# Optimization experiments

Measured on AMD Instinct MI355X. Metric: run time of the kernel, lower is better.

Reference implementation:

```python
import jax, jax.numpy as jnp
import numpy as np

NG, NR, C = 50000, 12000, 128     # lane nodes, roi nodes, n_map
NS = 6                            # num_scales
EPS, ELR, E1, E2 = 50000, 5000, 150000, 150000
GN_EPS = 1e-5


def gn(x, sb):
    # GroupNorm(num_groups=1) on [N, C]: normalize over C per row (biased var)
    m = x.mean(-1, keepdims=True)
    v = x.var(-1, keepdims=True)
    return (x - m) / jnp.sqrt(v + GN_EPS) * sb[0] + sb[1]


def lane_pooling(ctx_feat, ctx_pose, tgt_feat, tgt_pose, hi, wi,
                 input_w, relpose_w, relpose_b, ctx1_w, ctx1_gn, ctx2_w,
                 mlp1_w, mlp1_gn, mlp2_w, mlp2_gn, norm_gn):
    dist_feat = jax.nn.relu((ctx_pose[hi] - tgt_pose[wi]) @ relpose_w.T + relpose_b)  # [E,128]
    ctx = jnp.concatenate([ctx_feat[hi], dist_feat], -1)                               # [E,256]
    ctx = jax.nn.relu(gn(ctx @ ctx1_w.T, ctx1_gn)) @ ctx2_w.T                          # [E,128]
    identity = tgt_feat
    t = tgt_feat @ input_w.T
    t = t.at[wi].add(ctx)                 # scatter-reduce onto target nodes
    t = jax.nn.relu(gn(t, norm_gn))
    t = jax.nn.relu(gn(t @ mlp1_w.T, mlp1_gn))
    t = gn(t @ mlp2_w.T, mlp2_gn)
    return jax.nn.relu(t + identity)


def global_graph(feat, ps_u, ps_v, lr_u, lr_v,
                 ctr_w, ps_w, left_w, right_w, norm_gn, ctr2_w, ctr2_gn):
    res = feat
    for i in range(4):  # 4 fusion layers (structurally distinct weights)
        temp = feat @ ctr_w[i].T
        for k in range(2 * NS):  # pre0..pre5, suc0..suc5
            temp = temp.at[ps_u[k]].add(feat[ps_v[k]] @ ps_w[i, k].T)
        temp = temp.at[lr_u[0]].add(feat[lr_v[0]] @ left_w[i].T)
        temp = temp.at[lr_u[1]].add(feat[lr_v[1]] @ right_w[i].T)
        feat = jax.nn.relu(gn(temp, norm_gn[i]))
        feat = gn(feat @ ctr2_w[i].T, ctr2_gn[i])
        feat = jax.nn.relu(feat + res)
        res = feat
    return feat


def _gn_pack(key, lead):
    k1, k2 = jax.random.split(key)
    scale = 1.0 + 0.1 * jax.random.normal(k1, lead + (C,), jnp.float32)
    bias = 0.1 * jax.random.normal(k2, lead + (C,), jnp.float32)
    return jnp.stack([scale, bias], axis=-2)  # [..., 2, C]


def setup_inputs() -> dict:
    key = jax.random.key(0)
    ks = jax.random.split(key, 32)
    w = lambda k, sh: 0.05 * jax.random.normal(k, sh, jnp.float32)
    inp = {
        'roi_feat': jax.random.normal(ks[0], (NR, C), jnp.float32),
        'graph_pose': jax.random.normal(ks[1], (NG, 4), jnp.float32),
        'roi_pose': jax.random.normal(ks[2], (NR, 4), jnp.float32),
        'lp_input_w': w(ks[3], (2, C, C)),
        'lp_relpose_w': w(ks[4], (2, C, 4)),
        'lp_relpose_b': w(ks[5], (2, C)),
        'lp_ctx1_w': w(ks[6], (2, C, 2 * C)),
        'lp_ctx1_gn': _gn_pack(ks[7], (2,)),
        'lp_ctx2_w': w(ks[8], (2, C, C)),
        'lp_mlp1_w': w(ks[9], (2, C, C)),
        'lp_mlp1_gn': _gn_pack(ks[10], (2,)),
        'lp_mlp2_w': w(ks[11], (2, C, C)),
        'lp_mlp2_gn': _gn_pack(ks[12], (2,)),
        'lp_norm_gn': _gn_pack(ks[13], (2,)),
        'fuse_ctr_w': w(ks[14], (4, C, C)),
        'fuse_ps_w': w(ks[15], (4, 2 * NS, C, C)),
        'fuse_left_w': w(ks[16], (4, C, C)),
        'fuse_right_w': w(ks[17], (4, C, C)),
        'fuse_norm_gn': _gn_pack(ks[18], (4,)),
        'fuse_ctr2_w': w(ks[19], (4, C, C)),
        'fuse_ctr2_gn': _gn_pack(ks[20], (4,)),
        'e1_hi': jax.random.randint(ks[21], (E1,), 0, NR, jnp.int32),
        'e1_wi': jax.random.randint(ks[22], (E1,), 0, NG, jnp.int32),
        'e2_hi': jax.random.randint(ks[23], (E2,), 0, NG, jnp.int32),
        'e2_wi': jax.random.randint(ks[24], (E2,), 0, NR, jnp.int32),
        'ps_u': jax.random.randint(ks[25], (2 * NS, EPS), 0, NG, jnp.int32),
        'ps_v': jax.random.randint(ks[26], (2 * NS, EPS), 0, NG, jnp.int32),
        'lr_u': jax.random.randint(ks[27], (2, ELR), 0, NG, jnp.int32),
        'lr_v': jax.random.randint(ks[28], (2, ELR), 0, NG, jnp.int32),
    }
    return inp


def reference(roi_feat, graph_pose, roi_pose, lp_input_w, lp_relpose_w, lp_relpose_b,
              lp_ctx1_w, lp_ctx1_gn, lp_ctx2_w, lp_mlp1_w, lp_mlp1_gn, lp_mlp2_w,
              lp_mlp2_gn, lp_norm_gn, fuse_ctr_w, fuse_ps_w, fuse_left_w, fuse_right_w,
              fuse_norm_gn, fuse_ctr2_w, fuse_ctr2_gn, e1_hi, e1_wi, e2_hi, e2_wi,
              ps_u, ps_v, lr_u, lr_v):
    lp = lambda j: (lp_input_w[j], lp_relpose_w[j], lp_relpose_b[j], lp_ctx1_w[j],
                    lp_ctx1_gn[j], lp_ctx2_w[j], lp_mlp1_w[j], lp_mlp1_gn[j],
                    lp_mlp2_w[j], lp_mlp2_gn[j], lp_norm_gn[j])
    graph_feat = jnp.zeros((NG, C), jnp.float32)
    # roi2graph: context = roi, target = graph
    graph_feat = lane_pooling(roi_feat, roi_pose, graph_feat, graph_pose, e1_hi, e1_wi, *lp(0))
    graph_feat = global_graph(graph_feat, ps_u, ps_v, lr_u, lr_v,
                              fuse_ctr_w, fuse_ps_w, fuse_left_w, fuse_right_w,
                              fuse_norm_gn, fuse_ctr2_w, fuse_ctr2_gn)
    # graph2roi: context = graph, target = roi
    out = lane_pooling(graph_feat, graph_pose, roi_feat, roi_pose, e2_hi, e2_wi, *lp(1))
    return out
```

## Files before the change

kernel.cpp:

```cpp
#include <hip/hip_runtime.h>

#define NG 50000
#define NR 12000
#define EPS_N 50000
#define ELR_N 5000
#define E1_N 150000
#define E2_N 150000
#define GN_EPS_F 1e-5f
#define SCAN_CHUNK 4096
#define WST 136

typedef __attribute__((ext_vector_type(8))) __bf16 bf16x8;
typedef __attribute__((ext_vector_type(4))) float f32x4;

__device__ __forceinline__ bf16x8 cvt8(const float* __restrict__ p) {
    float4 x0 = *reinterpret_cast<const float4*>(p);
    float4 x1 = *reinterpret_cast<const float4*>(p + 4);
    bf16x8 a;
    a[0] = (__bf16)x0.x; a[1] = (__bf16)x0.y; a[2] = (__bf16)x0.z; a[3] = (__bf16)x0.w;
    a[4] = (__bf16)x1.x; a[5] = (__bf16)x1.y; a[6] = (__bf16)x1.z; a[7] = (__bf16)x1.w;
    return a;
}

struct PrepTab { const float* src[80]; int stride[80]; int n; };

__global__ void prepw_k(PrepTab tab, __bf16* __restrict__ wbuf)
{
    int t = blockIdx.x * 256 + threadIdx.x;
    int w = t >> 11;
    if (w >= tab.n) return;
    int rr = t & 2047;
    int chunk = rr >> 6, l = rr & 63;
    int wn = chunk >> 4, ks = (chunk >> 2) & 3, ni = chunk & 3;
    int c = wn * 64 + ni * 16 + (l & 15);
    int kb = (ks * 4 + (l >> 4)) * 8;
    const float* s = tab.src[w] + (size_t)c * tab.stride[w] + kb;
    bf16x8 o;
    #pragma unroll
    for (int e = 0; e < 8; ++e) o[e] = (__bf16)s[e];
    *reinterpret_cast<bf16x8*>(wbuf + (size_t)w * 16384 + rr * 8) = o;
}

__global__ void hist14_k(const int* __restrict__ ps_u, const int* __restrict__ lr_u,
                         int* __restrict__ cnt)
{
    int t = blockIdx.x * 256 + threadIdx.x;
    const int total = 12 * EPS_N + 2 * ELR_N;
    if (t >= total) return;
    int k, u;
    if (t < 12 * EPS_N) { k = t / EPS_N; u = ps_u[t]; }
    else { int r = t - 12 * EPS_N; k = 12 + r / ELR_N; u = lr_u[r]; }
    atomicAdd(&cnt[k * NG + u], 1);
}

__global__ void fill14_k(const int* __restrict__ ps_u, const int* __restrict__ ps_v,
                         const int* __restrict__ lr_u, const int* __restrict__ lr_v,
                         int* __restrict__ head, int* __restrict__ col)
{
    int t = blockIdx.x * 256 + threadIdx.x;
    const int total = 12 * EPS_N + 2 * ELR_N;
    if (t >= total) return;
    int k, u, v;
    if (t < 12 * EPS_N) { k = t / EPS_N; u = ps_u[t]; v = ps_v[t]; }
    else { int r = t - 12 * EPS_N; k = 12 + r / ELR_N; u = lr_u[r]; v = lr_v[r]; }
    int pos = atomicAdd(&head[k * NG + u], 1);
    col[pos] = v;
}

__global__ void histE_k(const int* __restrict__ wi, int n, int* __restrict__ cnt)
{
    int t = blockIdx.x * 256 + threadIdx.x;
    if (t >= n) return;
    atomicAdd(&cnt[wi[t]], 1);
}

__global__ void fillE_k(const int* __restrict__ wi, int n,
                        int* __restrict__ head, int* __restrict__ col)
{
    int t = blockIdx.x * 256 + threadIdx.x;
    if (t >= n) return;
    int pos = atomicAdd(&head[wi[t]], 1);
    col[pos] = t;
}

__global__ void scan1_k(const int* __restrict__ in, int n, int* __restrict__ bsum)
{
    __shared__ int sm[4];
    int base = blockIdx.x * SCAN_CHUNK;
    int s = 0;
    for (int i = threadIdx.x; i < SCAN_CHUNK; i += 256) {
        int idx = base + i;
        s += (idx < n) ? in[idx] : 0;
    }
    #pragma unroll
    for (int off = 1; off < 64; off <<= 1) s += __shfl_xor(s, off);
    if ((threadIdx.x & 63) == 0) sm[threadIdx.x >> 6] = s;
    __syncthreads();
    if (threadIdx.x == 0) bsum[blockIdx.x] = sm[0] + sm[1] + sm[2] + sm[3];
}

__global__ void scan2_k(int* __restrict__ bsum, int nb)
{
    if (threadIdx.x == 0) {
        int acc = 0;
        for (int i = 0; i < nb; ++i) { int t = bsum[i]; bsum[i] = acc; acc += t; }
    }
}

__global__ void scan3_k(const int* __restrict__ in, int n,
                        const int* __restrict__ bsum, int* __restrict__ outp)
{
    __shared__ int sm[256];
    int base = blockIdx.x * SCAN_CHUNK;
    int loc[16]; int s = 0;
    #pragma unroll
    for (int i = 0; i < 16; ++i) {
        int idx = base + threadIdx.x * 16 + i;
        loc[i] = (idx < n) ? in[idx] : 0; s += loc[i];
    }
    sm[threadIdx.x] = s; __syncthreads();
    for (int off = 1; off < 256; off <<= 1) {
        int v = (threadIdx.x >= off) ? sm[threadIdx.x - off] : 0;
        __syncthreads();
        sm[threadIdx.x] += v;
        __syncthreads();
    }
    int tp = (threadIdx.x ? sm[threadIdx.x - 1] : 0) + bsum[blockIdx.x];
    #pragma unroll
    for (int i = 0; i < 16; ++i) {
        int idx = base + threadIdx.x * 16 + i;
        if (idx < n) outp[idx] = tp;
        tp += loc[i];
        if (idx == n - 1) outp[n] = tp;
    }
}


__device__ __forceinline__ void mfma16(f32x4 (&acc)[8], const bf16x8 (&a)[4],
                                       const __bf16* __restrict__ gw, int lane)
{
    const __bf16* gwb = gw + lane * 8;
    #pragma unroll
    for (int ks = 0; ks < 4; ++ks) {
        #pragma unroll
        for (int n2 = 0; n2 < 8; ++n2) {
            const int chunk = (n2 >> 2) * 16 + ks * 4 + (n2 & 3);
            bf16x8 b = *reinterpret_cast<const bf16x8*>(gwb + chunk * 512);
            acc[n2] = __builtin_amdgcn_mfma_f32_16x16x32_bf16(a[ks], b, acc[n2], 0, 0, 0);
        }
    }
}

__device__ __forceinline__ void ss_to_frags(const float (&ss)[32], bf16x8 (&a)[4])
{
    #pragma unroll
    for (int ks = 0; ks < 4; ++ks)
        #pragma unroll
        for (int i = 0; i < 8; ++i)
            a[ks][i] = (__bf16)ss[ks * 8 + i];
}

__device__ __forceinline__ void gn_mi(const f32x4 (&acc)[8], float (&m)[4], float (&inv)[4])
{
    #pragma unroll
    for (int reg = 0; reg < 4; ++reg) {
        float s = 0.f, q = 0.f;
        #pragma unroll
        for (int n2 = 0; n2 < 8; ++n2) { float v = acc[n2][reg]; s += v; q = fmaf(v, v, q); }
        #pragma unroll
        for (int off = 1; off < 16; off <<= 1) {
            s += __shfl_xor(s, off);
            q += __shfl_xor(q, off);
        }
        m[reg] = s * (1.f / 128.f);
        inv[reg] = rsqrtf(fmaxf(q * (1.f / 128.f) - m[reg] * m[reg], 0.f) + GN_EPS_F);
    }
}

__device__ __forceinline__ void gn_relayout(const f32x4 (&acc)[8], const float* __restrict__ sb,
                                            __bf16* wl, bf16x8 (&a)[4], int r16, int kq)
{
    float m[4], inv[4];
    gn_mi(acc, m, inv);
    #pragma unroll
    for (int reg = 0; reg < 4; ++reg) {
        #pragma unroll
        for (int n2 = 0; n2 < 8; ++n2) {
            const int colc = n2 * 16 + r16;
            float y = (acc[n2][reg] - m[reg]) * inv[reg] * sb[colc] + sb[128 + colc];
            wl[(kq * 4 + reg) * WST + colc] = (__bf16)fmaxf(y, 0.f);
        }
    }
    #pragma unroll
    for (int ks = 0; ks < 4; ++ks)
        a[ks] = *reinterpret_cast<const bf16x8*>(wl + r16 * WST + ks * 32 + kq * 8);
}

template<typename CT>
__launch_bounds__(128, 3)
__global__ void edgefull_k(const int* __restrict__ hi_idx, const int* __restrict__ wi_idx,
                           const CT* __restrict__ ctxfeat,
                           const float* __restrict__ cpose, const float* __restrict__ tpose,
                           const float* __restrict__ rpw, const float* __restrict__ rpb,
                           const __bf16* __restrict__ wc1A, const __bf16* __restrict__ wc1B,
                           const float* __restrict__ sb,
                           __bf16* __restrict__ hout, int M)
{
    __shared__ float rw[640];
    const int tid = threadIdx.x, lane = tid & 63, wv = tid >> 6;
    const int r16 = lane & 15, kq = lane >> 4;
    const int wbase = blockIdx.x * 32 + wv * 16;
    const int erow = wbase + r16;
    const int ec = erow < M ? erow : M - 1;

    for (int i = tid; i < 640; i += 128)
        rw[i] = (i < 512) ? rpw[i] : rpb[i - 512];
    __syncthreads();

    const int hi = hi_idx[ec], wi = wi_idx[ec];
    float4 cp = *reinterpret_cast<const float4*>(cpose + (size_t)hi * 4);
    float4 tp = *reinterpret_cast<const float4*>(tpose + (size_t)wi * 4);
    const float d0 = cp.x - tp.x, d1 = cp.y - tp.y, d2 = cp.z - tp.z, d3 = cp.w - tp.w;

    f32x4 acc[8];
    #pragma unroll
    for (int n2 = 0; n2 < 8; ++n2) acc[n2] = (f32x4){0.f, 0.f, 0.f, 0.f};

    {
        bf16x8 a[4];
        const CT* sp = ctxfeat + (size_t)hi * 128 + kq * 8;
        #pragma unroll
        for (int ks = 0; ks < 4; ++ks) {
            if constexpr (sizeof(CT) == 4) a[ks] = cvt8((const float*)sp + ks * 32);
            else a[ks] = *reinterpret_cast<const bf16x8*>((const __bf16*)sp + ks * 32);
        }
        mfma16(acc, a, wc1A, lane);
    }
    {
        bf16x8 a[4];
        #pragma unroll
        for (int ks = 0; ks < 4; ++ks)
            #pragma unroll
            for (int i = 0; i < 8; ++i) {
                const int k = ks * 32 + kq * 8 + i;
                float4 w4 = *reinterpret_cast<const float4*>(&rw[k * 4]);
                float d = fmaf(d0, w4.x, fmaf(d1, w4.y, fmaf(d2, w4.z,
                          fmaf(d3, w4.w, rw[512 + k]))));
                a[ks][i] = (__bf16)fmaxf(d, 0.f);
            }
        mfma16(acc, a, wc1B, lane);
    }

    float m[4], inv[4];
    gn_mi(acc, m, inv);
    #pragma unroll
    for (int reg = 0; reg < 4; ++reg) {
        const int crow = wbase + kq * 4 + reg;
        if (crow < M) {
            __bf16* dp = hout + (size_t)crow * 128 + r16;
            #pragma unroll
            for (int n2 = 0; n2 < 8; ++n2) {
                const int colc = n2 * 16 + r16;
                float y = (acc[n2][reg] - m[reg]) * inv[reg] * sb[colc] + sb[128 + colc];
                dp[n2 * 16] = (__bf16)fmaxf(y, 0.f);
            }
        }
    }
}

struct FW { const __bf16* w[16]; };

__launch_bounds__(128, 3)
__global__ void fusedlayer_k(const __bf16* __restrict__ feat,
                             const int* __restrict__ rp, const int* __restrict__ col,
                             FW fw, const float* __restrict__ gn1,
                             const float* __restrict__ gn2,
                             __bf16* __restrict__ outp, int M)
{
    __shared__ __bf16 wl[2][16 * WST];
    const int tid = threadIdx.x, lane = tid & 63, wv = tid >> 6;
    const int r16 = lane & 15, kq = lane >> 4;
    const int wbase = blockIdx.x * 32 + wv * 16;
    const int wrow = (wbase + r16) < M ? (wbase + r16) : M - 1;

    f32x4 acc[8];
    #pragma unroll
    for (int n2 = 0; n2 < 8; ++n2) acc[n2] = (f32x4){0.f, 0.f, 0.f, 0.f};

    #pragma unroll
    for (int j = 0; j < 15; ++j) {
        float ss[32];
        #pragma unroll
        for (int i = 0; i < 32; ++i) ss[i] = 0.f;
        if (j == 14) {
            const __bf16* sp = feat + (size_t)wrow * 128 + kq * 8;
            #pragma unroll
            for (int ks = 0; ks < 4; ++ks) {
                bf16x8 h = *reinterpret_cast<const bf16x8*>(sp + ks * 32);
                #pragma unroll
                for (int i = 0; i < 8; ++i) ss[ks * 8 + i] = (float)h[i];
            }
        } else {
            const int b = rp[j * M + wrow], e = rp[j * M + wrow + 1];
            for (int t2 = b; t2 < e; ++t2) {
                const __bf16* sp = feat + (size_t)col[t2] * 128 + kq * 8;
                #pragma unroll
                for (int ks = 0; ks < 4; ++ks) {
                    bf16x8 h = *reinterpret_cast<const bf16x8*>(sp + ks * 32);
                    #pragma unroll
                    for (int i = 0; i < 8; ++i) ss[ks * 8 + i] += (float)h[i];
                }
            }
        }
        bf16x8 a[4];
        ss_to_frags(ss, a);
        mfma16(acc, a, fw.w[j], lane);
    }

    bf16x8 a2[4];
    gn_relayout(acc, gn1, wl[wv], a2, r16, kq);
    f32x4 acc2[8];
    #pragma unroll
    for (int n2 = 0; n2 < 8; ++n2) acc2[n2] = (f32x4){0.f, 0.f, 0.f, 0.f};
    mfma16(acc2, a2, fw.w[15], lane);

    float m[4], inv[4];
    gn_mi(acc2, m, inv);
    #pragma unroll
    for (int reg = 0; reg < 4; ++reg) {
        const int crow = wbase + kq * 4 + reg;
        if (crow < M) {
            __bf16* dp = outp + (size_t)crow * 128 + r16;
            const __bf16* rs = feat + (size_t)crow * 128 + r16;
            #pragma unroll
            for (int n2 = 0; n2 < 8; ++n2) {
                const int colc = n2 * 16 + r16;
                float y = (acc2[n2][reg] - m[reg]) * inv[reg] * gn2[colc] + gn2[128 + colc];
                y += (float)rs[n2 * 16];
                dp[n2 * 16] = (__bf16)fmaxf(y, 0.f);
            }
        }
    }
}

template<bool LP2>
__launch_bounds__(128, 3)
__global__ void lptail_k(const __bf16* __restrict__ hsrc,
                         const int* __restrict__ rp, const int* __restrict__ col,
                         const float* __restrict__ roi,
                         const __bf16* __restrict__ wc2, const __bf16* __restrict__ winW,
                         const __bf16* __restrict__ wm1, const __bf16* __restrict__ wm2,
                         const float* __restrict__ ngn, const float* __restrict__ m1gn,
                         const float* __restrict__ m2gn,
                         void* __restrict__ outp, int M)
{
    __shared__ __bf16 wl[2][16 * WST];
    const int tid = threadIdx.x, lane = tid & 63, wv = tid >> 6;
    const int r16 = lane & 15, kq = lane >> 4;
    const int wbase = blockIdx.x * 32 + wv * 16;
    const int wrow = (wbase + r16) < M ? (wbase + r16) : M - 1;

    f32x4 acc[8];
    #pragma unroll
    for (int n2 = 0; n2 < 8; ++n2) acc[n2] = (f32x4){0.f, 0.f, 0.f, 0.f};

    {
        float ss[32];
        #pragma unroll
        for (int i = 0; i < 32; ++i) ss[i] = 0.f;
        const int b = rp[wrow], e = rp[wrow + 1];
        for (int t2 = b; t2 < e; ++t2) {
            const __bf16* sp = hsrc + (size_t)col[t2] * 128 + kq * 8;
            #pragma unroll
            for (int ks = 0; ks < 4; ++ks) {
                bf16x8 h = *reinterpret_cast<const bf16x8*>(sp + ks * 32);
                #pragma unroll
                for (int i = 0; i < 8; ++i) ss[ks * 8 + i] += (float)h[i];
            }
        }
        bf16x8 a[4];
        ss_to_frags(ss, a);
        mfma16(acc, a, wc2, lane);
    }
    if (LP2) {
        bf16x8 a[4];
        const float* sp = roi + (size_t)wrow * 128 + kq * 8;
        #pragma unroll
        for (int ks = 0; ks < 4; ++ks) a[ks] = cvt8(sp + ks * 32);
        mfma16(acc, a, winW, lane);
    }

    {
        bf16x8 a[4];
        gn_relayout(acc, ngn, wl[wv], a, r16, kq);
        #pragma unroll
        for (int n2 = 0; n2 < 8; ++n2) acc[n2] = (f32x4){0.f, 0.f, 0.f, 0.f};
        mfma16(acc, a, wm1, lane);
    }
    {
        bf16x8 a[4];
        gn_relayout(acc, m1gn, wl[wv], a, r16, kq);
        #pragma unroll
        for (int n2 = 0; n2 < 8; ++n2) acc[n2] = (f32x4){0.f, 0.f, 0.f, 0.f};
        mfma16(acc, a, wm2, lane);
    }

    float m[4], inv[4];
    gn_mi(acc, m, inv);
    #pragma unroll
    for (int reg = 0; reg < 4; ++reg) {
        const int crow = wbase + kq * 4 + reg;
        if (crow < M) {
            #pragma unroll
            for (int n2 = 0; n2 < 8; ++n2) {
                const int colc = n2 * 16 + r16;
                float y = (acc[n2][reg] - m[reg]) * inv[reg] * m2gn[colc] + m2gn[128 + colc];
                if (LP2) {
                    y += roi[(size_t)crow * 128 + colc];
                    ((float*)outp)[(size_t)crow * 128 + colc] = fmaxf(y, 0.f);
                } else {
                    ((__bf16*)outp)[(size_t)crow * 128 + colc] = (__bf16)fmaxf(y, 0.f);
                }
            }
        }
    }
}

extern "C" void kernel_launch(void* const* d_in, const int* in_sizes, int n_in,
                              void* d_out, int out_size, void* d_ws, size_t ws_size,
                              hipStream_t stream)
{
    const float* roi_feat   = (const float*)d_in[0];
    const float* graph_pose = (const float*)d_in[1];
    const float* roi_pose   = (const float*)d_in[2];
    const float* lp_input_w = (const float*)d_in[3];
    const float* lp_rpw     = (const float*)d_in[4];
    const float* lp_rpb     = (const float*)d_in[5];
    const float* lp_c1w     = (const float*)d_in[6];
    const float* lp_c1gn    = (const float*)d_in[7];
    const float* lp_c2w     = (const float*)d_in[8];
    const float* lp_m1w     = (const float*)d_in[9];
    const float* lp_m1gn    = (const float*)d_in[10];
    const float* lp_m2w     = (const float*)d_in[11];
    const float* lp_m2gn    = (const float*)d_in[12];
    const float* lp_ngn     = (const float*)d_in[13];
    const float* f_ctrw     = (const float*)d_in[14];
    const float* f_psw      = (const float*)d_in[15];
    const float* f_lw       = (const float*)d_in[16];
    const float* f_rw       = (const float*)d_in[17];
    const float* f_ngn      = (const float*)d_in[18];
    const float* f_c2w      = (const float*)d_in[19];
    const float* f_c2gn     = (const float*)d_in[20];
    const int* e1_hi = (const int*)d_in[21];
    const int* e1_wi = (const int*)d_in[22];
    const int* e2_hi = (const int*)d_in[23];
    const int* e2_wi = (const int*)d_in[24];
    const int* ps_u  = (const int*)d_in[25];
    const int* ps_v  = (const int*)d_in[26];
    const int* lr_u  = (const int*)d_in[27];
    const int* lr_v  = (const int*)d_in[28];
    float* out = (float*)d_out;

    __bf16* gA   = (__bf16*)d_ws;
    __bf16* gB   = gA + (size_t)NG * 128;
    __bf16* hbuf = gB + (size_t)NG * 128;
    __bf16* wbuf = hbuf + (size_t)E1_N * 128;
    int* ip      = (int*)(wbuf + (size_t)80 * 16384);
    int* cnt14   = ip;             ip += 14 * NG;
    int* rp14    = ip;             ip += 14 * NG + 1;
    int* col14   = ip;             ip += 12 * EPS_N + 2 * ELR_N;
    int* cntE1   = ip;             ip += NG;
    int* rpE1    = ip;             ip += NG + 1;
    int* colE1   = ip;             ip += E1_N;
    int* cntE2   = ip;             ip += NR;
    int* rpE2    = ip;             ip += NR + 1;
    int* colE2   = ip;             ip += E2_N;
    int* bsum    = ip;             ip += 256;

    dim3 blk(256), blk128(128);
    const dim3 gNG32((NG + 31) / 32), gNR32((NR + 31) / 32), gE32((E1_N + 31) / 32);
    const int NE14 = 12 * EPS_N + 2 * ELR_N;
    const dim3 gH14((NE14 + 255) / 256);

    PrepTab tab; int nw = 0;
    auto addw = [&](const float* p, int s) { tab.src[nw] = p; tab.stride[nw] = s; ++nw; };
    addw(lp_c1w, 256);
    addw(lp_c1w + 128, 256);
    addw(lp_c1w + 32768, 256);
    addw(lp_c1w + 32768 + 128, 256);
    addw(lp_input_w + 16384, 128);
    addw(lp_c2w, 128); addw(lp_c2w + 16384, 128);
    addw(lp_m1w, 128); addw(lp_m1w + 16384, 128);
    addw(lp_m2w, 128); addw(lp_m2w + 16384, 128);
    for (int i = 0; i < 4; ++i) addw(f_ctrw + (size_t)i * 16384, 128);
    for (int i = 0; i < 4; ++i)
        for (int k = 0; k < 12; ++k) addw(f_psw + ((size_t)i * 12 + k) * 16384, 128);
    for (int i = 0; i < 4; ++i) addw(f_lw + (size_t)i * 16384, 128);
    for (int i = 0; i < 4; ++i) addw(f_rw + (size_t)i * 16384, 128);
    for (int i = 0; i < 4; ++i) addw(f_c2w + (size_t)i * 16384, 128);
    tab.n = nw;
    auto wb = [&](int idx) { return (const __bf16*)(wbuf + (size_t)idx * 16384); };
    prepw_k<<<dim3((nw * 2048 + 255) / 256), blk, 0, stream>>>(tab, wbuf);

    hipMemsetAsync(cnt14, 0, (size_t)14 * NG * 4, stream);
    hist14_k<<<gH14, blk, 0, stream>>>(ps_u, lr_u, cnt14);
    {
        int n = 14 * NG, nb = (n + SCAN_CHUNK - 1) / SCAN_CHUNK;
        scan1_k<<<nb, blk, 0, stream>>>(cnt14, n, bsum);
        scan2_k<<<1, blk, 0, stream>>>(bsum, nb);
        scan3_k<<<nb, blk, 0, stream>>>(cnt14, n, bsum, rp14);
    }
    hipMemcpyAsync(cnt14, rp14, (size_t)14 * NG * 4, hipMemcpyDeviceToDevice, stream);
    fill14_k<<<gH14, blk, 0, stream>>>(ps_u, ps_v, lr_u, lr_v, cnt14, col14);

    hipMemsetAsync(cntE1, 0, (size_t)NG * 4, stream);
    histE_k<<<(E1_N + 255) / 256, blk, 0, stream>>>(e1_wi, E1_N, cntE1);
    {
        int n = NG, nb = (n + SCAN_CHUNK - 1) / SCAN_CHUNK;
        scan1_k<<<nb, blk, 0, stream>>>(cntE1, n, bsum);
        scan2_k<<<1, blk, 0, stream>>>(bsum, nb);
        scan3_k<<<nb, blk, 0, stream>>>(cntE1, n, bsum, rpE1);
    }
    hipMemcpyAsync(cntE1, rpE1, (size_t)NG * 4, hipMemcpyDeviceToDevice, stream);
    fillE_k<<<(E1_N + 255) / 256, blk, 0, stream>>>(e1_wi, E1_N, cntE1, colE1);

    hipMemsetAsync(cntE2, 0, (size_t)NR * 4, stream);
    histE_k<<<(E2_N + 255) / 256, blk, 0, stream>>>(e2_wi, E2_N, cntE2);
    {
        int n = NR, nb = (n + SCAN_CHUNK - 1) / SCAN_CHUNK;
        scan1_k<<<nb, blk, 0, stream>>>(cntE2, n, bsum);
        scan2_k<<<1, blk, 0, stream>>>(bsum, nb);
        scan3_k<<<nb, blk, 0, stream>>>(cntE2, n, bsum, rpE2);
    }
    hipMemcpyAsync(cntE2, rpE2, (size_t)NR * 4, hipMemcpyDeviceToDevice, stream);
    fillE_k<<<(E2_N + 255) / 256, blk, 0, stream>>>(e2_wi, E2_N, cntE2, colE2);

    edgefull_k<float><<<gE32, blk128, 0, stream>>>(
        e1_hi, e1_wi, roi_feat, roi_pose, graph_pose, lp_rpw, lp_rpb,
        wb(0), wb(1), lp_c1gn, hbuf, E1_N);
    lptail_k<false><<<gNG32, blk128, 0, stream>>>(
        hbuf, rpE1, colE1, nullptr, wb(5), nullptr, wb(7), wb(9),
        lp_ngn, lp_m1gn, lp_m2gn, gA, NG);

    for (int i = 0; i < 4; ++i) {
        FW fw;
        for (int k = 0; k < 12; ++k) fw.w[k] = wb(15 + i * 12 + k);
        fw.w[12] = wb(63 + i); fw.w[13] = wb(67 + i);
        fw.w[14] = wb(11 + i); fw.w[15] = wb(71 + i);
        const __bf16* src = (i & 1) ? gB : gA;
        __bf16* dst = (i & 1) ? gA : gB;
        fusedlayer_k<<<gNG32, blk128, 0, stream>>>(
            src, rp14, col14, fw, f_ngn + (size_t)i * 256,
            f_c2gn + (size_t)i * 256, dst, NG);
    }

    edgefull_k<__bf16><<<gE32, blk128, 0, stream>>>(
        e2_hi, e2_wi, gA, graph_pose, roi_pose, lp_rpw + 512, lp_rpb + 128,
        wb(2), wb(3), lp_c1gn + 256, hbuf, E2_N);
    lptail_k<true><<<gNR32, blk128, 0, stream>>>(
        hbuf, rpE2, colE2, roi_feat, wb(6), wb(4), wb(8), wb(10),
        lp_ngn + 256, lp_m1gn + 256, lp_m2gn + 256, out, NR);
}
```

Before: 697.3 us.

## Split fused-layer scale work across two waves per 16-row tile

Each block of fusedlayer_k now handles 16 rows instead of 32. The two waves split the 15 gather+MFMA scales between them (7 and 8) and reduce their partial accumulators through shared memory. The second GEMM is split by output-column halves across the waves, and the GroupNorm statistics are combined via shared memory. Occupancy is raised to 4 blocks per SIMD and the grid is doubled. The aim is more parallelism and latency hiding for the gather-heavy loop, at the cost of extra syncs, shared-memory traffic and an unbalanced split between the waves.

```diff
diff --git a/kernel.cpp b/kernel.cpp
--- a/kernel.cpp
+++ b/kernel.cpp
@@ -135,7 +135,6 @@
     }
 }
 
-
 __device__ __forceinline__ void mfma16(f32x4 (&acc)[8], const bf16x8 (&a)[4],
                                        const __bf16* __restrict__ gw, int lane)
 {
@@ -270,25 +269,26 @@
 
 struct FW { const __bf16* w[16]; };
 
-__launch_bounds__(128, 3)
+__launch_bounds__(128, 4)
 __global__ void fusedlayer_k(const __bf16* __restrict__ feat,
                              const int* __restrict__ rp, const int* __restrict__ col,
                              FW fw, const float* __restrict__ gn1,
                              const float* __restrict__ gn2,
                              __bf16* __restrict__ outp, int M)
 {
-    __shared__ __bf16 wl[2][16 * WST];
+    __shared__ float red[64 * 36];
+    __shared__ __bf16 atile[16 * WST];
+    __shared__ float smS[2][16], smQ[2][16];
     const int tid = threadIdx.x, lane = tid & 63, wv = tid >> 6;
     const int r16 = lane & 15, kq = lane >> 4;
-    const int wbase = blockIdx.x * 32 + wv * 16;
+    const int wbase = blockIdx.x * 16;
     const int wrow = (wbase + r16) < M ? (wbase + r16) : M - 1;
 
     f32x4 acc[8];
     #pragma unroll
     for (int n2 = 0; n2 < 8; ++n2) acc[n2] = (f32x4){0.f, 0.f, 0.f, 0.f};
 
-    #pragma unroll
-    for (int j = 0; j < 15; ++j) {
+    auto DO_SCALE = [&](int j) {
         float ss[32];
         #pragma unroll
         for (int i = 0; i < 32; ++i) ss[i] = 0.f;
@@ -315,29 +315,98 @@
         bf16x8 a[4];
         ss_to_frags(ss, a);
         mfma16(acc, a, fw.w[j], lane);
-    }
-
-    bf16x8 a2[4];
-    gn_relayout(acc, gn1, wl[wv], a2, r16, kq);
-    f32x4 acc2[8];
-    #pragma unroll
-    for (int n2 = 0; n2 < 8; ++n2) acc2[n2] = (f32x4){0.f, 0.f, 0.f, 0.f};
-    mfma16(acc2, a2, fw.w[15], lane);
-
-    float m[4], inv[4];
-    gn_mi(acc2, m, inv);
-    #pragma unroll
-    for (int reg = 0; reg < 4; ++reg) {
-        const int crow = wbase + kq * 4 + reg;
-        if (crow < M) {
-            __bf16* dp = outp + (size_t)crow * 128 + r16;
-            const __bf16* rs = feat + (size_t)crow * 128 + r16;
+    };
+
+    if (wv == 0) {
+        #pragma unroll
+        for (int j = 0; j < 7; ++j) DO_SCALE(j);
+    } else {
+        #pragma unroll
+        for (int j = 7; j < 15; ++j) DO_SCALE(j);
+        #pragma unroll
+        for (int n2 = 0; n2 < 8; ++n2)
+            *reinterpret_cast<f32x4*>(&red[lane * 36 + n2 * 4]) = acc[n2];
+    }
+    __syncthreads();
+
+    if (wv == 0) {
+        #pragma unroll
+        for (int n2 = 0; n2 < 8; ++n2) {
+            f32x4 r = *reinterpret_cast<const f32x4*>(&red[lane * 36 + n2 * 4]);
+            acc[n2][0] += r[0]; acc[n2][1] += r[1]; acc[n2][2] += r[2]; acc[n2][3] += r[3];
+        }
+        float m[4], inv[4];
+        gn_mi(acc, m, inv);
+        #pragma unroll
+        for (int reg = 0; reg < 4; ++reg) {
             #pragma unroll
             for (int n2 = 0; n2 < 8; ++n2) {
                 const int colc = n2 * 16 + r16;
-                float y = (acc2[n2][reg] - m[reg]) * inv[reg] * gn2[colc] + gn2[128 + colc];
-                y += (float)rs[n2 * 16];
-                dp[n2 * 16] = (__bf16)fmaxf(y, 0.f);
+                float y = (acc[n2][reg] - m[reg]) * inv[reg] * gn1[colc] + gn1[128 + colc];
+                atile[(kq * 4 + reg) * WST + colc] = (__bf16)fmaxf(y, 0.f);
+            }
+        }
+    }
+    __syncthreads();
+
+    bf16x8 a2[4];
+    #pragma unroll
+    for (int ks = 0; ks < 4; ++ks)
+        a2[ks] = *reinterpret_cast<const bf16x8*>(atile + r16 * WST + ks * 32 + kq * 8);
+    f32x4 acc2[4];
+    #pragma unroll
+    for (int ni = 0; ni < 4; ++ni) acc2[ni] = (f32x4){0.f, 0.f, 0.f, 0.f};
+    {
+        const __bf16* gwb = fw.w[15] + ((size_t)wv << 13) + lane * 8;
+        #pragma unroll
+        for (int ks = 0; ks < 4; ++ks) {
+            #pragma unroll
+            for (int ni = 0; ni < 4; ++ni) {
+                bf16x8 b = *reinterpret_cast<const bf16x8*>(gwb + (ks * 4 + ni) * 512);
+                acc2[ni] = __builtin_amdgcn_mfma_f32_16x16x32_bf16(a2[ks], b, acc2[ni], 0, 0, 0);
+            }
+        }
+    }
+
+    float ps[4], pq[4];
+    #pragma unroll
+    for (int reg = 0; reg < 4; ++reg) {
+        float s = 0.f, q = 0.f;
+        #pragma unroll
+        for (int ni = 0; ni < 4; ++ni) { float v = acc2[ni][reg]; s += v; q = fmaf(v, v, q); }
+        #pragma unroll
+        for (int off = 1; off < 16; off <<= 1) {
+            s += __shfl_xor(s, off);
+            q += __shfl_xor(q, off);
+        }
+        ps[reg] = s; pq[reg] = q;
+    }
+    if (r16 == 0) {
+        #pragma unroll
+        for (int reg = 0; reg < 4; ++reg) {
+            smS[wv][kq * 4 + reg] = ps[reg];
+            smQ[wv][kq * 4 + reg] = pq[reg];
+        }
+    }
+    __syncthreads();
+
+    #pragma unroll
+    for (int reg = 0; reg < 4; ++reg) {
+        const int lr = kq * 4 + reg;
+        const float S = smS[0][lr] + smS[1][lr];
+        const float Q = smQ[0][lr] + smQ[1][lr];
+        const float m = S * (1.f / 128.f);
+        const float inv = rsqrtf(fmaxf(Q * (1.f / 128.f) - m * m, 0.f) + GN_EPS_F);
+        const int crow = wbase + lr;
+        if (crow < M) {
+            __bf16* dp = outp + (size_t)crow * 128 + wv * 64 + r16;
+            const __bf16* rs = feat + (size_t)crow * 128 + wv * 64 + r16;
+            #pragma unroll
+            for (int ni = 0; ni < 4; ++ni) {
+                const int colc = wv * 64 + ni * 16 + r16;
+                float y = (acc2[ni][reg] - m) * inv * gn2[colc] + gn2[128 + colc];
+                y += (float)rs[ni * 16];
+                dp[ni * 16] = (__bf16)fmaxf(y, 0.f);
             }
         }
     }
@@ -478,7 +547,8 @@
     int* bsum    = ip;             ip += 256;
 
     dim3 blk(256), blk128(128);
-    const dim3 gNG32((NG + 31) / 32), gNR32((NR + 31) / 32), gE32((E1_N + 31) / 32);
+    const dim3 gNG16((NG + 15) / 16), gNG32((NG + 31) / 32),
+               gNR32((NR + 31) / 32), gE32((E1_N + 31) / 32);
     const int NE14 = 12 * EPS_N + 2 * ELR_N;
     const dim3 gH14((NE14 + 255) / 256);
 
@@ -549,7 +619,7 @@
         fw.w[14] = wb(11 + i); fw.w[15] = wb(71 + i);
         const __bf16* src = (i & 1) ? gB : gA;
         __bf16* dst = (i & 1) ? gA : gB;
-        fusedlayer_k<<<gNG32, blk128, 0, stream>>>(
+        fusedlayer_k<<<gNG16, blk128, 0, stream>>>(
             src, rp14, col14, fw, f_ngn + (size_t)i * 256,
             f_c2gn + (size_t)i * 256, dst, NG);
     }
```

New measurement: 707.4 us. No clear change (+1.5%).

## Software-pipeline neighbor row gathers in fused graph layer and unroll pooling gather

Applied to the files above, without the earlier changes.

In the fused global-graph layer, the CSR offsets for all 14 edge types are loaded up front. The first two neighbor rows of the next edge type are prefetched into double-buffered registers while the current type's MFMA runs, with any extra neighbors handled in a fallback loop. The launch bound is lowered from 3 to 2 blocks per SM to make room for the extra registers, and the lane-pooling gather loop is unrolled by two so two row loads are in flight at once. This targets gather latency stalls but may reduce occupancy.

```diff
diff --git a/kernel.cpp b/kernel.cpp
--- a/kernel.cpp
+++ b/kernel.cpp
@@ -135,7 +135,6 @@
     }
 }
 
-
 __device__ __forceinline__ void mfma16(f32x4 (&acc)[8], const bf16x8 (&a)[4],
                                        const __bf16* __restrict__ gw, int lane)
 {
@@ -270,7 +269,7 @@
 
 struct FW { const __bf16* w[16]; };
 
-__launch_bounds__(128, 3)
+__launch_bounds__(128, 2)
 __global__ void fusedlayer_k(const __bf16* __restrict__ feat,
                              const int* __restrict__ rp, const int* __restrict__ col,
                              FW fw, const float* __restrict__ gn1,
@@ -283,26 +282,57 @@
     const int wbase = blockIdx.x * 32 + wv * 16;
     const int wrow = (wbase + r16) < M ? (wbase + r16) : M - 1;
 
+    int beg[14], deg[14];
+    #pragma unroll
+    for (int j = 0; j < 14; ++j) {
+        beg[j] = rp[j * M + wrow];
+        deg[j] = rp[j * M + wrow + 1] - beg[j];
+    }
+
     f32x4 acc[8];
     #pragma unroll
     for (int n2 = 0; n2 < 8; ++n2) acc[n2] = (f32x4){0.f, 0.f, 0.f, 0.f};
 
+    auto LDROW = [&](int row, bf16x8 (&h)[4]) {
+        const __bf16* sp = feat + (size_t)row * 128 + kq * 8;
+        #pragma unroll
+        for (int ks = 0; ks < 4; ++ks)
+            h[ks] = *reinterpret_cast<const bf16x8*>(sp + ks * 32);
+    };
+
+    bf16x8 hc0[2][4], hc1[2][4];
+    int c0n, c1n;
+    {
+        int c00 = (deg[0] > 0) ? col[beg[0]] : wrow;
+        int c10 = (deg[0] > 1) ? col[beg[0] + 1] : wrow;
+        LDROW(c00, hc0[0]);
+        LDROW(c10, hc1[0]);
+        c0n = (deg[1] > 0) ? col[beg[1]] : wrow;
+        c1n = (deg[1] > 1) ? col[beg[1] + 1] : wrow;
+    }
+
     #pragma unroll
     for (int j = 0; j < 15; ++j) {
+        const int cur = j & 1, nxt = cur ^ 1;
+        if (j < 14) { LDROW(c0n, hc0[nxt]); LDROW(c1n, hc1[nxt]); }
+        if (j + 2 < 14) {
+            c0n = (deg[j + 2] > 0) ? col[beg[j + 2]] : wrow;
+            c1n = (deg[j + 2] > 1) ? col[beg[j + 2] + 1] : wrow;
+        } else if (j + 2 == 14) {
+            c0n = wrow; c1n = wrow;
+        }
+        const float f0 = (j == 14) ? 1.f : (deg[j] > 0 ? 1.f : 0.f);
+        const float f1 = (j == 14) ? 0.f : (deg[j] > 1 ? 1.f : 0.f);
         float ss[32];
         #pragma unroll
-        for (int i = 0; i < 32; ++i) ss[i] = 0.f;
-        if (j == 14) {
-            const __bf16* sp = feat + (size_t)wrow * 128 + kq * 8;
-            #pragma unroll
-            for (int ks = 0; ks < 4; ++ks) {
-                bf16x8 h = *reinterpret_cast<const bf16x8*>(sp + ks * 32);
-                #pragma unroll
-                for (int i = 0; i < 8; ++i) ss[ks * 8 + i] = (float)h[i];
-            }
-        } else {
-            const int b = rp[j * M + wrow], e = rp[j * M + wrow + 1];
-            for (int t2 = b; t2 < e; ++t2) {
+        for (int ks = 0; ks < 4; ++ks)
+            #pragma unroll
+            for (int i = 0; i < 8; ++i)
+                ss[ks * 8 + i] = fmaf(f0, (float)hc0[cur][ks][i],
+                                      f1 * (float)hc1[cur][ks][i]);
+        if (j < 14 && deg[j] > 2) {
+            const int b = beg[j], e = beg[j] + deg[j];
+            for (int t2 = b + 2; t2 < e; ++t2) {
                 const __bf16* sp = feat + (size_t)col[t2] * 128 + kq * 8;
                 #pragma unroll
                 for (int ks = 0; ks < 4; ++ks) {
@@ -369,7 +399,24 @@
         #pragma unroll
         for (int i = 0; i < 32; ++i) ss[i] = 0.f;
         const int b = rp[wrow], e = rp[wrow + 1];
-        for (int t2 = b; t2 < e; ++t2) {
+        int t2 = b;
+        for (; t2 + 2 <= e; t2 += 2) {
+            const int ca = col[t2], cb = col[t2 + 1];
+            const __bf16* spa = hsrc + (size_t)ca * 128 + kq * 8;
+            const __bf16* spb = hsrc + (size_t)cb * 128 + kq * 8;
+            bf16x8 ha[4], hb[4];
+            #pragma unroll
+            for (int ks = 0; ks < 4; ++ks) {
+                ha[ks] = *reinterpret_cast<const bf16x8*>(spa + ks * 32);
+                hb[ks] = *reinterpret_cast<const bf16x8*>(spb + ks * 32);
+            }
+            #pragma unroll
+            for (int ks = 0; ks < 4; ++ks)
+                #pragma unroll
+                for (int i = 0; i < 8; ++i)
+                    ss[ks * 8 + i] += (float)ha[ks][i] + (float)hb[ks][i];
+        }
+        for (; t2 < e; ++t2) {
             const __bf16* sp = hsrc + (size_t)col[t2] * 128 + kq * 8;
             #pragma unroll
             for (int ks = 0; ks < 4; ++ks) {
```

After: 867.9 us. 1.24x slower.
